# Kernel tuning notes

Measured on AMD Instinct MI355X. Metric: run time of the kernel, lower is better.

Reference implementation:

```python
import jax, jax.numpy as jnp
import numpy as np

N = 30000   # vertices
E = 4000    # hyperedges
NNZ = 960000
D = 256
ALPHA = 0.1
BETA = 0.8


def setup_inputs() -> dict:
    key = jax.random.key(0)
    k1, k2, k3, k4, k5, k6 = jax.random.split(key, 6)
    X = jax.random.normal(k1, (N, D), dtype=jnp.float32)
    X0 = jax.random.normal(k2, (N, D), dtype=jnp.float32)
    H = jax.random.uniform(k3, (N, E), dtype=jnp.float32)
    vertex = jax.random.randint(k4, (NNZ,), 0, N, dtype=jnp.int64)
    edges = jax.random.randint(k5, (NNZ,), 0, E, dtype=jnp.int64)
    # Linear(in_features=256, out_features=256, bias=False) weight, torch layout [out, in]
    W = jax.random.normal(k6, (D, D), dtype=jnp.float32) * (1.0 / np.sqrt(D))
    return {"X": X, "X0": X0, "H": H, "W": W, "vertex": vertex, "edges": edges}


def reference(X, X0, H, W, vertex, edges):
    # degree scalings from dense incidence matrix
    degV = jnp.sum(H, axis=1) ** -0.5            # [N]
    degV = jnp.where(jnp.isinf(degV), 1.0, degV)[:, None]
    degE = (jnp.sum(H, axis=0) ** -0.5)[:, None]  # [E,1]

    Xve = X[vertex]                               # [nnz, d] gather
    # scatter-mean to edges
    sums = jax.ops.segment_sum(Xve, edges, num_segments=E)            # [E, d]
    cnt = jax.ops.segment_sum(jnp.ones((Xve.shape[0],), X.dtype), edges, num_segments=E)
    Xe = sums / jnp.maximum(cnt, 1.0)[:, None]
    Xe = Xe * degE

    Xev = Xe[edges]                               # [nnz, d] gather
    Xv = jax.ops.segment_sum(Xev, vertex, num_segments=X.shape[0])    # [N, d]
    Xv = Xv * degV

    Xi = (1.0 - ALPHA) * Xv + ALPHA * X0
    out = (1.0 - BETA) * Xi + BETA * (Xi @ W.T)
    return out
```

## Files before the change

### kernel.cpp

```cpp
#include <hip/hip_runtime.h>

#define D 256
#define ALPHA 0.1f
#define BETA 0.8f
#define CAPE 320
#define CAPV 64

typedef float v4f __attribute__((ext_vector_type(4)));

__device__ __forceinline__ void add4(float4& a, const float4& b) {
    a.x += b.x; a.y += b.y; a.z += b.z; a.w += b.w;
}

__device__ __forceinline__ unsigned short f2bf(float f) {
    unsigned int u = __float_as_uint(f);
    u += 0x7FFFu + ((u >> 16) & 1u);
    return (unsigned short)(u >> 16);
}
__device__ __forceinline__ float bf2f(unsigned short h) {
    return __uint_as_float((unsigned int)h << 16);
}
__device__ __forceinline__ void addbf4(float4& a, const ushort4& t) {
    a.x += bf2f(t.x); a.y += bf2f(t.y); a.z += bf2f(t.z); a.w += bf2f(t.w);
}

__global__ __launch_bounds__(256) void k_init(const float* __restrict__ W,
                                              float* __restrict__ Wt,
                                              float* __restrict__ colsum,
                                              int* __restrict__ cnt_e,
                                              int* __restrict__ cnt_v,
                                              int n, int e) {
    int idx = blockIdx.x * 256 + threadIdx.x;
    if (idx < D * D) {
        int o = idx >> 8, i = idx & 255;
        Wt[i * D + o] = BETA * W[o * D + i] + ((i == o) ? (1.0f - BETA) : 0.0f);
    }
    if (idx < e) { colsum[idx] = 0.f; cnt_e[idx] = 0; }
    if (idx < n) cnt_v[idx] = 0;
}

__global__ __launch_bounds__(256) void k_build(const float* __restrict__ H,
                                               float* __restrict__ rowsum,
                                               float* __restrict__ colsum,
                                               const int* __restrict__ vertex,
                                               const int* __restrict__ edges,
                                               int* __restrict__ cnt_e,
                                               int* __restrict__ cnt_v,
                                               unsigned short* __restrict__ list_e,
                                               unsigned short* __restrict__ list_v,
                                               const float* __restrict__ X,
                                               unsigned short* __restrict__ Xb,
                                               int n, int e, int nnz,
                                               int nPair, int total4) {
    const int tid = threadIdx.x;
    const int b   = blockIdx.x;

    if (b >= 2 * nPair) {
        int idx = (b - 2 * nPair) * 256 + tid;
        if (idx < total4) {
            float4 x = reinterpret_cast<const float4*>(X)[idx];
            ushort4 o;
            o.x = f2bf(x.x); o.y = f2bf(x.y); o.z = f2bf(x.z); o.w = f2bf(x.w);
            reinterpret_cast<ushort4*>(Xb)[idx] = o;
        }
        return;
    }

    if ((b & 1) == 0) {
        const int rid  = b >> 1;
        const int wave = tid >> 6, lane = tid & 63;
        const int ec4  = e >> 2;
        __shared__ float4 sl[2][1000];

        float4 cp[16];
        #pragma unroll
        for (int k = 0; k < 16; ++k) cp[k] = make_float4(0.f, 0.f, 0.f, 0.f);

        const int rbase = rid * 32 + wave * 8;
        for (int i = 0; i < 8; ++i) {
            int row = rbase + i;
            float rs = 0.f;
            if (row < n) {
                const v4f* Hr = reinterpret_cast<const v4f*>(H + (size_t)row * e);
                float4 v[16];
                #pragma unroll
                for (int k = 0; k < 16; ++k) {
                    int s = lane + 64 * k;
                    if (s < ec4) {
                        v4f t = __builtin_nontemporal_load(Hr + s);
                        v[k] = make_float4(t.x, t.y, t.z, t.w);
                    } else {
                        v[k] = make_float4(0.f, 0.f, 0.f, 0.f);
                    }
                }
                #pragma unroll
                for (int k = 0; k < 16; ++k) {
                    rs += (v[k].x + v[k].y) + (v[k].z + v[k].w);
                    add4(cp[k], v[k]);
                }
            }
            #pragma unroll
            for (int s = 32; s > 0; s >>= 1) rs += __shfl_down(rs, s, 64);
            if (lane == 0 && row < n) rowsum[row] = rs;
        }

        if (wave < 2) {
            #pragma unroll
            for (int k = 0; k < 16; ++k) {
                int s = lane + 64 * k;
                if (s < ec4) sl[wave][s] = cp[k];
            }
        }
        __syncthreads();
        if (wave >= 2) {
            #pragma unroll
            for (int k = 0; k < 16; ++k) {
                int s = lane + 64 * k;
                if (s < ec4) add4(sl[wave - 2][s], cp[k]);
            }
        }
        __syncthreads();

        for (int c4 = tid; c4 < ec4; c4 += 256) {
            float4 s = sl[0][c4];
            add4(s, sl[1][c4]);
            atomicAdd(&colsum[4 * c4 + 0], s.x);
            atomicAdd(&colsum[4 * c4 + 1], s.y);
            atomicAdd(&colsum[4 * c4 + 2], s.z);
            atomicAdd(&colsum[4 * c4 + 3], s.w);
        }
    } else {
        const int fid = b >> 1;
        int base4 = ((fid * 256) + tid) * 4;
        if (base4 + 3 < nnz) {
            int4 ee = reinterpret_cast<const int4*>(edges)[base4 >> 2];
            int4 vv = reinterpret_cast<const int4*>(vertex)[base4 >> 2];
            int p0 = atomicAdd(&cnt_e[ee.x], 1);
            int p1 = atomicAdd(&cnt_e[ee.y], 1);
            int p2 = atomicAdd(&cnt_e[ee.z], 1);
            int p3 = atomicAdd(&cnt_e[ee.w], 1);
            int q0 = atomicAdd(&cnt_v[vv.x], 1);
            int q1 = atomicAdd(&cnt_v[vv.y], 1);
            int q2 = atomicAdd(&cnt_v[vv.z], 1);
            int q3 = atomicAdd(&cnt_v[vv.w], 1);
            if (p0 < CAPE) list_e[(size_t)ee.x * CAPE + p0] = (unsigned short)vv.x;
            if (p1 < CAPE) list_e[(size_t)ee.y * CAPE + p1] = (unsigned short)vv.y;
            if (p2 < CAPE) list_e[(size_t)ee.z * CAPE + p2] = (unsigned short)vv.z;
            if (p3 < CAPE) list_e[(size_t)ee.w * CAPE + p3] = (unsigned short)vv.w;
            if (q0 < CAPV) list_v[(size_t)vv.x * CAPV + q0] = (unsigned short)ee.x;
            if (q1 < CAPV) list_v[(size_t)vv.y * CAPV + q1] = (unsigned short)ee.y;
            if (q2 < CAPV) list_v[(size_t)vv.z * CAPV + q2] = (unsigned short)ee.z;
            if (q3 < CAPV) list_v[(size_t)vv.w * CAPV + q3] = (unsigned short)ee.w;
        } else {
            for (int i = base4; i < nnz; ++i) {
                int ee = edges[i], v = vertex[i];
                int p = atomicAdd(&cnt_e[ee], 1);
                if (p < CAPE) list_e[(size_t)ee * CAPE + p] = (unsigned short)v;
                int q = atomicAdd(&cnt_v[v], 1);
                if (q < CAPV) list_v[(size_t)v * CAPV + q] = (unsigned short)ee;
            }
        }
    }
}

__global__ __launch_bounds__(256) void k_edge_agg(const unsigned short* __restrict__ Xb,
                                                  const unsigned short* __restrict__ list_e,
                                                  const int* __restrict__ cnt_e,
                                                  const float* __restrict__ colsum,
                                                  unsigned short* __restrict__ Xeb, int e) {
    const int eid  = blockIdx.x * 4 + (threadIdx.x >> 6);
    const int lane = threadIdx.x & 63;
    if (eid >= e) return;
    const int cnt  = cnt_e[eid];
    const int m    = cnt < CAPE ? cnt : CAPE;
    const int j0   = eid * CAPE;

    float4 a[8];
    #pragma unroll
    for (int k = 0; k < 8; ++k) a[k] = make_float4(0.f, 0.f, 0.f, 0.f);

    int j = 0;
    for (; j + 7 < m; j += 8) {
        #pragma unroll
        for (int k = 0; k < 8; ++k) {
            int v = list_e[j0 + j + k];
            ushort4 t = reinterpret_cast<const ushort4*>(Xb + (size_t)v * D)[lane];
            addbf4(a[k], t);
        }
    }
    for (; j < m; ++j) {
        int v = list_e[j0 + j];
        ushort4 t = reinterpret_cast<const ushort4*>(Xb + (size_t)v * D)[lane];
        addbf4(a[0], t);
    }
    #pragma unroll
    for (int k = 1; k < 8; ++k) add4(a[0], a[k]);

    float scale = rsqrtf(colsum[eid]) / (float)(cnt > 0 ? cnt : 1);
    ushort4 o;
    o.x = f2bf(a[0].x * scale); o.y = f2bf(a[0].y * scale);
    o.z = f2bf(a[0].z * scale); o.w = f2bf(a[0].w * scale);
    reinterpret_cast<ushort4*>(Xeb + (size_t)eid * D)[lane] = o;
}

__global__ __launch_bounds__(256) void k_vertex_agg(const unsigned short* __restrict__ Xeb,
                                                    const unsigned short* __restrict__ list_v,
                                                    const int* __restrict__ cnt_v,
                                                    const float* __restrict__ rowsum,
                                                    const float* __restrict__ X0,
                                                    float* __restrict__ Xi, int n) {
    const int v    = blockIdx.x * 4 + (threadIdx.x >> 6);
    const int lane = threadIdx.x & 63;
    if (v >= n) return;
    const int cnt  = cnt_v[v];
    const int m    = cnt < CAPV ? cnt : CAPV;
    const int j0   = v * CAPV;

    float4 a[4];
    #pragma unroll
    for (int k = 0; k < 4; ++k) a[k] = make_float4(0.f, 0.f, 0.f, 0.f);

    int j = 0;
    for (; j + 3 < m; j += 4) {
        #pragma unroll
        for (int k = 0; k < 4; ++k) {
            int e = list_v[j0 + j + k];
            ushort4 t = reinterpret_cast<const ushort4*>(Xeb + (size_t)e * D)[lane];
            addbf4(a[k], t);
        }
    }
    for (; j < m; ++j) {
        int e = list_v[j0 + j];
        ushort4 t = reinterpret_cast<const ushort4*>(Xeb + (size_t)e * D)[lane];
        addbf4(a[0], t);
    }
    add4(a[0], a[1]); add4(a[2], a[3]); add4(a[0], a[2]);

    float rs = rowsum[v];
    float degV = (rs > 0.f) ? rsqrtf(rs) : 1.0f;
    float scale = (1.0f - ALPHA) * degV;
    float4 x0 = reinterpret_cast<const float4*>(X0 + (size_t)v * D)[lane];
    float4 o;
    o.x = scale * a[0].x + ALPHA * x0.x;
    o.y = scale * a[0].y + ALPHA * x0.y;
    o.z = scale * a[0].z + ALPHA * x0.z;
    o.w = scale * a[0].w + ALPHA * x0.w;
    reinterpret_cast<float4*>(Xi + (size_t)v * D)[lane] = o;
}

__global__ __launch_bounds__(256) void k_gemm(const float* __restrict__ A,
                                              const float* __restrict__ B,
                                              float* __restrict__ C, int n) {
    const int BM = 128, BN = 128, BK = 16;
    __shared__ float As[BK][BM + 4];
    __shared__ float Bs[BK][BN];
    const int row0 = blockIdx.x * BM;
    const int col0 = blockIdx.y * BN;
    const int tid = threadIdx.x;
    const int tx = tid & 15, ty = tid >> 4;

    float c[8][8];
    #pragma unroll
    for (int i = 0; i < 8; ++i)
        #pragma unroll
        for (int j = 0; j < 8; ++j) c[i][j] = 0.f;

    for (int kk = 0; kk < D; kk += BK) {
        #pragma unroll
        for (int h = 0; h < 2; ++h) {
            int idx = tid + h * 256;
            int r = idx >> 2, cq = idx & 3;
            int row = row0 + r;
            float4 a = (row < n)
                ? reinterpret_cast<const float4*>(A + (size_t)row * D + kk)[cq]
                : make_float4(0.f, 0.f, 0.f, 0.f);
            As[cq * 4 + 0][r] = a.x;
            As[cq * 4 + 1][r] = a.y;
            As[cq * 4 + 2][r] = a.z;
            As[cq * 4 + 3][r] = a.w;
        }
        #pragma unroll
        for (int h = 0; h < 2; ++h) {
            int idx = tid + h * 256;
            int k = idx >> 5, c4 = idx & 31;
            float4 b = reinterpret_cast<const float4*>(B + (size_t)(kk + k) * D + col0)[c4];
            reinterpret_cast<float4*>(&Bs[k][c4 * 4])[0] = b;
        }
        __syncthreads();
        #pragma unroll
        for (int k = 0; k < BK; ++k) {
            float4 a0 = *reinterpret_cast<const float4*>(&As[k][ty * 8]);
            float4 a1 = *reinterpret_cast<const float4*>(&As[k][ty * 8 + 4]);
            float4 b0 = *reinterpret_cast<const float4*>(&Bs[k][tx * 8]);
            float4 b1 = *reinterpret_cast<const float4*>(&Bs[k][tx * 8 + 4]);
            float av[8] = {a0.x, a0.y, a0.z, a0.w, a1.x, a1.y, a1.z, a1.w};
            float bv[8] = {b0.x, b0.y, b0.z, b0.w, b1.x, b1.y, b1.z, b1.w};
            #pragma unroll
            for (int i = 0; i < 8; ++i)
                #pragma unroll
                for (int j = 0; j < 8; ++j)
                    c[i][j] = fmaf(av[i], bv[j], c[i][j]);
        }
        __syncthreads();
    }
    #pragma unroll
    for (int i = 0; i < 8; ++i) {
        int row = row0 + ty * 8 + i;
        if (row < n) {
            float4 o0 = make_float4(c[i][0], c[i][1], c[i][2], c[i][3]);
            float4 o1 = make_float4(c[i][4], c[i][5], c[i][6], c[i][7]);
            float4* p = reinterpret_cast<float4*>(C + (size_t)row * D + col0 + tx * 8);
            p[0] = o0; p[1] = o1;
        }
    }
}

extern "C" void kernel_launch(void* const* d_in, const int* in_sizes, int n_in,
                              void* d_out, int out_size, void* d_ws, size_t ws_size,
                              hipStream_t stream) {
    const float* X      = (const float*)d_in[0];
    const float* X0     = (const float*)d_in[1];
    const float* H      = (const float*)d_in[2];
    const float* W      = (const float*)d_in[3];
    const int*   vertex = (const int*)d_in[4];
    const int*   edges  = (const int*)d_in[5];
    float* out = (float*)d_out;

    const int n   = in_sizes[0] / D;
    const int e   = in_sizes[2] / n;
    const int nnz = in_sizes[4];

    char* base = (char*)d_ws;
    size_t off = 0;
    auto carve = [&](size_t bytes) {
        size_t o = off;
        off += (bytes + 255) & ~(size_t)255;
        return o;
    };
    float*          Xi     = (float*)(base + carve((size_t)n * D * 4));
    unsigned short* Xb     = (unsigned short*)(base + carve((size_t)n * D * 2));
    unsigned short* Xeb    = (unsigned short*)(base + carve((size_t)e * D * 2));
    float*          Wt     = (float*)(base + carve((size_t)D * D * 4));
    float*          rowsum = (float*)(base + carve((size_t)n * 4));
    float*          colsum = (float*)(base + carve((size_t)e * 4));
    int*            cnt_e  = (int*)(base + carve((size_t)e * 4));
    int*            cnt_v  = (int*)(base + carve((size_t)n * 4));
    unsigned short* list_e = (unsigned short*)(base + carve((size_t)e * CAPE * 2));
    unsigned short* list_v = (unsigned short*)(base + carve((size_t)n * CAPV * 2));
    (void)ws_size; (void)n_in; (void)out_size;

    const int nRowBlk  = (n + 31) / 32;
    const int nPair    = nRowBlk;
    const int total4   = n * D / 4;
    const int nConvBlk = (total4 + 255) / 256;

    k_init<<<dim3(256), dim3(256), 0, stream>>>(W, Wt, colsum, cnt_e, cnt_v, n, e);
    k_build<<<dim3(2 * nPair + nConvBlk), dim3(256), 0, stream>>>(
        H, rowsum, colsum, vertex, edges, cnt_e, cnt_v, list_e, list_v,
        X, Xb, n, e, nnz, nPair, total4);
    k_edge_agg<<<dim3((e + 3) / 4), dim3(256), 0, stream>>>(Xb, list_e, cnt_e, colsum, Xeb, e);
    k_vertex_agg<<<dim3((n + 3) / 4), dim3(256), 0, stream>>>(Xeb, list_v, cnt_v, rowsum, X0, Xi, n);
    k_gemm<<<dim3((n + 127) / 128, D / 128), dim3(256), 0, stream>>>(Xi, Wt, out, n);
}
```

Baseline: 348.4 us.

## Move vertex incidence-list construction into edge aggregation kernel to overlap work

The per-vertex CSR-like list construction (cnt_v atomics and list_v writes) moves out of k_build into k_edge_agg. There its blocks are interleaved with the edge-gather blocks. The aim is to shorten the atomic-heavy build phase and hide the vertex-list atomics behind the memory-bound edge gathers, since the edge aggregation does not depend on list_v. The cost is a more complex block-index mapping in k_edge_agg and possible contention between the two kinds of blocks.

```diff
diff --git a/kernel.cpp b/kernel.cpp
--- a/kernel.cpp
+++ b/kernel.cpp
@@ -45,9 +45,7 @@
                                                const int* __restrict__ vertex,
                                                const int* __restrict__ edges,
                                                int* __restrict__ cnt_e,
-                                               int* __restrict__ cnt_v,
                                                unsigned short* __restrict__ list_e,
-                                               unsigned short* __restrict__ list_v,
                                                const float* __restrict__ X,
                                                unsigned short* __restrict__ Xb,
                                                int n, int e, int nnz,
@@ -139,25 +137,15 @@
             int p1 = atomicAdd(&cnt_e[ee.y], 1);
             int p2 = atomicAdd(&cnt_e[ee.z], 1);
             int p3 = atomicAdd(&cnt_e[ee.w], 1);
-            int q0 = atomicAdd(&cnt_v[vv.x], 1);
-            int q1 = atomicAdd(&cnt_v[vv.y], 1);
-            int q2 = atomicAdd(&cnt_v[vv.z], 1);
-            int q3 = atomicAdd(&cnt_v[vv.w], 1);
             if (p0 < CAPE) list_e[(size_t)ee.x * CAPE + p0] = (unsigned short)vv.x;
             if (p1 < CAPE) list_e[(size_t)ee.y * CAPE + p1] = (unsigned short)vv.y;
             if (p2 < CAPE) list_e[(size_t)ee.z * CAPE + p2] = (unsigned short)vv.z;
             if (p3 < CAPE) list_e[(size_t)ee.w * CAPE + p3] = (unsigned short)vv.w;
-            if (q0 < CAPV) list_v[(size_t)vv.x * CAPV + q0] = (unsigned short)ee.x;
-            if (q1 < CAPV) list_v[(size_t)vv.y * CAPV + q1] = (unsigned short)ee.y;
-            if (q2 < CAPV) list_v[(size_t)vv.z * CAPV + q2] = (unsigned short)ee.z;
-            if (q3 < CAPV) list_v[(size_t)vv.w * CAPV + q3] = (unsigned short)ee.w;
         } else {
             for (int i = base4; i < nnz; ++i) {
                 int ee = edges[i], v = vertex[i];
                 int p = atomicAdd(&cnt_e[ee], 1);
                 if (p < CAPE) list_e[(size_t)ee * CAPE + p] = (unsigned short)v;
-                int q = atomicAdd(&cnt_v[v], 1);
-                if (q < CAPV) list_v[(size_t)v * CAPV + q] = (unsigned short)ee;
             }
         }
     }
@@ -167,9 +155,47 @@
                                                   const unsigned short* __restrict__ list_e,
                                                   const int* __restrict__ cnt_e,
                                                   const float* __restrict__ colsum,
-                                                  unsigned short* __restrict__ Xeb, int e) {
-    const int eid  = blockIdx.x * 4 + (threadIdx.x >> 6);
-    const int lane = threadIdx.x & 63;
+                                                  unsigned short* __restrict__ Xeb,
+                                                  const int* __restrict__ vertex,
+                                                  const int* __restrict__ edges,
+                                                  int* __restrict__ cnt_v,
+                                                  unsigned short* __restrict__ list_v,
+                                                  int e, int nnz, int nPairEA) {
+    const int b   = blockIdx.x;
+    const int tid = threadIdx.x;
+
+    int echunk = -1;
+    if (b < 2 * nPairEA) {
+        if (b & 1) {
+            const int fid = b >> 1;
+            int base4 = ((fid * 256) + tid) * 4;
+            if (base4 + 3 < nnz) {
+                int4 ee = reinterpret_cast<const int4*>(edges)[base4 >> 2];
+                int4 vv = reinterpret_cast<const int4*>(vertex)[base4 >> 2];
+                int q0 = atomicAdd(&cnt_v[vv.x], 1);
+                int q1 = atomicAdd(&cnt_v[vv.y], 1);
+                int q2 = atomicAdd(&cnt_v[vv.z], 1);
+                int q3 = atomicAdd(&cnt_v[vv.w], 1);
+                if (q0 < CAPV) list_v[(size_t)vv.x * CAPV + q0] = (unsigned short)ee.x;
+                if (q1 < CAPV) list_v[(size_t)vv.y * CAPV + q1] = (unsigned short)ee.y;
+                if (q2 < CAPV) list_v[(size_t)vv.z * CAPV + q2] = (unsigned short)ee.z;
+                if (q3 < CAPV) list_v[(size_t)vv.w * CAPV + q3] = (unsigned short)ee.w;
+            } else {
+                for (int i = base4; i < nnz; ++i) {
+                    int ee = edges[i], v = vertex[i];
+                    int q = atomicAdd(&cnt_v[v], 1);
+                    if (q < CAPV) list_v[(size_t)v * CAPV + q] = (unsigned short)ee;
+                }
+            }
+            return;
+        }
+        echunk = b >> 1;
+    } else {
+        echunk = b - nPairEA;
+    }
+
+    const int eid  = echunk * 4 + (tid >> 6);
+    const int lane = tid & 63;
     if (eid >= e) return;
     const int cnt  = cnt_e[eid];
     const int m    = cnt < CAPE ? cnt : CAPE;
@@ -353,12 +379,15 @@
     const int nPair    = nRowBlk;
     const int total4   = n * D / 4;
     const int nConvBlk = (total4 + 255) / 256;
+    const int nEa      = (e + 3) / 4;
+    const int nFv      = (nnz / 4 + 255) / 256;
+    const int nPairEA  = nFv;
 
     k_init<<<dim3(256), dim3(256), 0, stream>>>(W, Wt, colsum, cnt_e, cnt_v, n, e);
     k_build<<<dim3(2 * nPair + nConvBlk), dim3(256), 0, stream>>>(
-        H, rowsum, colsum, vertex, edges, cnt_e, cnt_v, list_e, list_v,
-        X, Xb, n, e, nnz, nPair, total4);
-    k_edge_agg<<<dim3((e + 3) / 4), dim3(256), 0, stream>>>(Xb, list_e, cnt_e, colsum, Xeb, e);
+        H, rowsum, colsum, vertex, edges, cnt_e, list_e, X, Xb, n, e, nnz, nPair, total4);
+    k_edge_agg<<<dim3(nEa + nFv), dim3(256), 0, stream>>>(
+        Xb, list_e, cnt_e, colsum, Xeb, vertex, edges, cnt_v, list_v, e, nnz, nPairEA);
     k_vertex_agg<<<dim3((n + 3) / 4), dim3(256), 0, stream>>>(Xeb, list_v, cnt_v, rowsum, X0, Xi, n);
     k_gemm<<<dim3((n + 127) / 128, D / 128), dim3(256), 0, stream>>>(Xi, Wt, out, n);
 }
```

New measurement: 349.0 us. About the same (+0.2%).
